# Kernel optimization log

Measured on AMD Instinct MI355X. Metric: run time of the kernel, lower is better.

Reference implementation:

```python
import jax, jax.numpy as jnp
import numpy as np

EPS = 1e-8
CUTOFF = 7.0
B, A, EPG = 128, 100, 2048
N, E = B * A, B * EPG
LAT, HID, FCH, NRBF, NTYPES, NT = 256, 128, 512, 16, 100, 50


def _lattice(lengths, angles):
    # pymatgen-style lattice_params_to_matrix; angles in degrees. -> [B,3,3] rows are a,b,c vectors
    a, b, c = lengths[:, 0], lengths[:, 1], lengths[:, 2]
    al, be, ga = (jnp.radians(angles[:, k]) for k in range(3))
    val = (jnp.cos(al) * jnp.cos(be) - jnp.cos(ga)) / (jnp.sin(al) * jnp.sin(be))
    gs = jnp.arccos(jnp.clip(val, -1.0, 1.0))
    z = jnp.zeros_like(a)
    va = jnp.stack([a * jnp.sin(be), z, a * jnp.cos(be)], -1)
    vb = jnp.stack([-b * jnp.sin(al) * jnp.cos(gs), b * jnp.sin(al) * jnp.sin(gs), b * jnp.cos(al)], -1)
    vc = jnp.stack([z, z, c], -1)
    return jnp.stack([va, vb, vc], 1)


def setup_inputs() -> dict:
    rng = np.random.default_rng(0)
    # sorted-per-graph edge list with i != j (so no_iden_mask is all-true)
    i = rng.integers(0, A, (B, EPG))
    j = (i + rng.integers(1, A, (B, EPG))) % A
    order = np.argsort(i * A + j, axis=1, kind='stable')
    i = np.take_along_axis(i, order, 1)
    j = np.take_along_axis(j, order, 1)
    goff = (np.arange(B) * A)[:, None]
    edge_index = np.stack([(j + goff).reshape(-1), (i + goff).reshape(-1)]).astype(np.int32)  # [2,E], row0=j(src), row1=i(dst)
    to_jimages = rng.integers(-1, 2, (E, 3)).astype(np.int32)
    batch = np.repeat(np.arange(B), A).astype(np.int32)
    num_atoms = np.full((B,), A, np.int32)
    atom_types = rng.integers(0, NTYPES, (N,)).astype(np.int32)
    time_steps = rng.integers(0, NT, (B,)).astype(np.int32)

    ks = jax.random.split(jax.random.key(0), 12)
    f32 = jnp.float32
    inp = dict(
        latents=jax.random.normal(ks[0], (B, LAT), f32),
        gt_frac_coords=jax.random.uniform(ks[1], (N, 3), f32),
        lengths=8.0 + 4.0 * jax.random.uniform(ks[2], (B, 3), f32),
        angles=90.0 + 8.0 * (jax.random.uniform(ks[3], (B, 3), f32) - 0.5),
        coord_noise=jax.random.normal(ks[4], (N, 3), f32),
        sigmas=jnp.exp(jnp.linspace(np.log(0.01), np.log(10.0), NT)).astype(f32),
        atom_emb=jax.random.normal(ks[5], (NTYPES, HID), f32),
        rbf_W=0.05 * jax.random.normal(ks[6], (NRBF, HID), f32),
        rbf_b=jnp.zeros((HID,), f32),
        bb_W=0.1 * jax.random.normal(ks[7], (HID, HID), f32),
        bb_b=jnp.zeros((HID,), f32),
        sc_W0=0.05 * jax.random.normal(ks[8], (LAT + HID, FCH), f32),
        sc_b0=jnp.zeros((FCH,), f32),
        sc_W1=0.05 * jax.random.normal(ks[9], (FCH, FCH), f32),
        sc_b1=jnp.zeros((FCH,), f32),
        sc_W2=0.05 * jax.random.normal(ks[10], (FCH, 1), f32),
        sc_b2=jnp.zeros((1,), f32),
        num_atoms=jnp.asarray(num_atoms),
        atom_types=jnp.asarray(atom_types),
        batch=jnp.asarray(batch),
        edge_index=jnp.asarray(edge_index),
        to_jimages=jnp.asarray(to_jimages),
        time_steps=jnp.asarray(time_steps),
    )
    return inp


def reference(latents, gt_frac_coords, lengths, angles, coord_noise, sigmas,
              atom_emb, rbf_W, rbf_b, bb_W, bb_b,
              sc_W0, sc_b0, sc_W1, sc_b1, sc_W2, sc_b2,
              num_atoms, atom_types, batch, edge_index, to_jimages, time_steps):
    seg_sum = jax.ops.segment_sum
    L = _lattice(lengths, angles)            # [B,3,3]
    Linv = jnp.linalg.inv(L)
    Ln, Lni = L[batch], Linv[batch]          # per-node lattice [N,3,3]
    cart_gt = jnp.einsum('ni,nij->nj', gt_frac_coords, Ln)
    sig_node = sigmas[time_steps][batch][:, None]              # [N,1]
    pert = cart_gt + sig_node * coord_noise
    # correct_cart_coords: wrap back into unit cell
    frac_p = jnp.einsum('ni,nij->nj', pert, Lni) % 1.0
    pert = jnp.einsum('ni,nij->nj', frac_p, Ln)
    jn, iN = edge_index[0], edge_index[1]
    offs = jnp.einsum('ei,eij->ej', to_jimages.astype(pert.dtype), L[batch[jn]])
    dvec = pert[iN] - pert[jn] - offs                           # [E,3]
    dist = jnp.linalg.norm(dvec, axis=-1)
    # backbone: atom-type embeddings + Gaussian RBF edge MLP -> [E,HID]
    mus = jnp.linspace(0.0, CUTOFF, rbf_W.shape[0]).astype(pert.dtype)
    rbf = jnp.exp(-10.0 * (dist[:, None] - mus) ** 2)
    h = atom_emb[atom_types]
    ef = jax.nn.silu((h[jn] + h[iN] + rbf @ rbf_W + rbf_b) @ bb_W + bb_b)
    # latents repeat_interleave(num_multi_edge_per_graph) == gather by edge's graph id
    ef = jnp.concatenate([ef, latents[batch[jn]]], axis=1)      # [E, HID+LAT]
    hh = jax.nn.relu(ef @ sc_W0 + sc_b0)
    hh = jax.nn.relu(hh @ sc_W1 + sc_b1)
    scores = hh @ sc_W2 + sc_b2                                 # [E,1]
    # align_gt_cart_coords: minimum-image gt coords relative to perturbed coords
    frac_gt = jnp.einsum('ni,nij->nj', cart_gt, Lni)
    fd = frac_gt - frac_p
    fd = fd - jnp.round(fd)
    aligned = pert + jnp.einsum('ni,nij->nj', fd, Ln)
    gt_dvec = aligned[iN] - aligned[jn] - offs
    gt_d = jnp.linalg.norm(gt_dvec, axis=-1, keepdims=True)
    pd = dist[:, None]
    gt_scores = gt_d - pd
    # per_node loss: group multi-edges by contiguous (i,j) runs
    start = jnp.concatenate([jnp.ones((1,), bool), (iN[1:] != iN[:-1]) | (jn[1:] != jn[:-1])])
    seg = jnp.cumsum(start.astype(jnp.int32)) - 1               # [E], < E segments
    cnt = seg_sum(jnp.ones((E,), pert.dtype), seg, num_segments=E)
    c = jnp.maximum(cnt, 1.0)
    sv = scores * dvec / (pd + EPS)
    gv = gt_scores * dvec / (pd + EPS)
    sE = seg_sum(sv, seg, num_segments=E) / c[:, None]
    gE = seg_sum(gv, seg, num_segments=E) / c[:, None]
    recv = jnp.round(seg_sum(iN.astype(pert.dtype), seg, num_segments=E) / c).astype(jnp.int32)
    sN = seg_sum(sE, recv, num_segments=N)                      # scores_per_node_pos [N,3]
    gN = seg_sum(gE, recv, num_segments=N)
    sq = (sN - gN / sig_node) ** 2
    na = num_atoms.astype(pert.dtype)[:, None]
    score_loss = (seg_sum(sq, batch, num_segments=B) / na).mean()
    # pbc symmetry regularizer
    preds = pert + sN / sig_node
    center = seg_sum(preds, batch, num_segments=B) / na
    dc = preds - center[batch]
    pbs = (jnp.abs(dc[:, 0].max() + dc[:, 0].min())
           + jnp.abs(dc[:, 1].max() + dc[:, 1].min())
           + jnp.abs(dc[:, 2].max() + dc[:, 2].min()))
    return (score_loss, pbs)
```

## Files before the change

### kernel.cpp

```cpp
#include <hip/hip_runtime.h>
#include <hip/hip_bf16.h>

namespace {
constexpr int Bb = 128, Nn = 12800, Ee = 262144;
constexpr int LAT = 256, HID = 128, FCH = 512, NRBF = 16;
constexpr int TE = 64;
constexpr int TSTRIDE = 1040;

constexpr int WS_L      = 0;
constexpr int WS_LI     = 1152;
constexpr int WS_SIG    = 2304;
constexpr int WS_RBFW2  = 2432;
constexpr int WS_CVEC   = 4480;
constexpr int WS_HB     = 4608;
constexpr int WS_LATP   = 17408;
constexpr int WS_PERT   = 82944;
constexpr int WS_ALIGN  = 121344;
constexpr int WS_SN     = 159744;
constexpr int WS_GN     = 198144;
constexpr int WS_PREDS  = 236544;
constexpr int WS_BSUM   = 274944;
constexpr int WS_CENTER = 275328;
constexpr int WS_MINMAX = 275712;
constexpr int WS_W0T_F  = 276000;
constexpr int WS_W1T_F  = 308768;
}

typedef short bf16x8 __attribute__((ext_vector_type(8)));
typedef float f32x4 __attribute__((ext_vector_type(4)));

static __device__ __forceinline__ unsigned short f2bf(float f) {
  unsigned int u = __float_as_uint(f);
  unsigned int r = (u + 0x7fffu + ((u >> 16) & 1u)) >> 16;
  return (unsigned short)r;
}
static __device__ __forceinline__ unsigned int pk2bf(float a, float b) {
  unsigned int r;
  asm("v_cvt_pk_bf16_f32 %0, %1, %2" : "=v"(r) : "v"(a), "v"(b));
  return r;
}
static __device__ __forceinline__ float fastrcp(float x) {
  return __builtin_amdgcn_rcpf(x);
}

static __device__ __forceinline__ void atomicMaxFloat(float* addr, float val) {
  int* ai = reinterpret_cast<int*>(addr);
  int old = *ai;
  while (__int_as_float(old) < val) {
    int assumed = old;
    old = atomicCAS(ai, assumed, __float_as_int(val));
    if (old == assumed) break;
  }
}
static __device__ __forceinline__ void atomicMinFloat(float* addr, float val) {
  int* ai = reinterpret_cast<int*>(addr);
  int old = *ai;
  while (__int_as_float(old) > val) {
    int assumed = old;
    old = atomicCAS(ai, assumed, __float_as_int(val));
    if (old == assumed) break;
  }
}

__global__ __launch_bounds__(256) void k_pre(
    const float* lengths, const float* angles, const float* sigmas, const int* tsteps,
    const float* aemb, const float* bbW, const float* rbfW, const float* rbfb,
    const float* bbb, const float* latents, const float* scW0, const float* scb0,
    const float* scW1, unsigned short* w0t, unsigned short* w1t, float* ws) {
  const int blk = blockIdx.x, t = threadIdx.x;
  if (blk < 304) {
    int gid = blk * 256 + t;
    if (gid < 2 * Nn * 3) ws[WS_SN + gid] = 0.f;
    else if (gid < 2 * Nn * 3 + 2 * Bb * 3) ws[WS_BSUM + (gid - 2 * Nn * 3)] = 0.f;
    else if (gid < 2 * Nn * 3 + 2 * Bb * 3 + 3) ws[WS_MINMAX + (gid - 2 * Nn * 3 - 2 * Bb * 3)] = -3.0e38f;
    else if (gid < 2 * Nn * 3 + 2 * Bb * 3 + 6) ws[WS_MINMAX + (gid - 2 * Nn * 3 - 2 * Bb * 3)] = 3.0e38f;
  } else if (blk == 304) {
    int b = t;
    if (b >= Bb) return;
    float a = lengths[b * 3 + 0], bl = lengths[b * 3 + 1], c = lengths[b * 3 + 2];
    const float d2r = 0.017453292519943295f;
    float al = angles[b * 3 + 0] * d2r, be = angles[b * 3 + 1] * d2r, ga = angles[b * 3 + 2] * d2r;
    float ca = cosf(al), cb = cosf(be), cg = cosf(ga), sa = sinf(al), sb = sinf(be);
    float val = (ca * cb - cg) / (sa * sb);
    val = fminf(1.f, fmaxf(-1.f, val));
    float gs = acosf(val);
    float L[3][3];
    L[0][0] = a * sb;              L[0][1] = 0.f;                L[0][2] = a * cb;
    L[1][0] = -bl * sa * cosf(gs); L[1][1] = bl * sa * sinf(gs); L[1][2] = bl * ca;
    L[2][0] = 0.f;                 L[2][1] = 0.f;                L[2][2] = c;
    float det = L[0][0] * (L[1][1] * L[2][2] - L[1][2] * L[2][1])
              - L[0][1] * (L[1][0] * L[2][2] - L[1][2] * L[2][0])
              + L[0][2] * (L[1][0] * L[2][1] - L[1][1] * L[2][0]);
    float id = 1.f / det;
    float inv[3][3];
    inv[0][0] =  (L[1][1]*L[2][2] - L[1][2]*L[2][1]) * id;
    inv[0][1] = -(L[0][1]*L[2][2] - L[0][2]*L[2][1]) * id;
    inv[0][2] =  (L[0][1]*L[1][2] - L[0][2]*L[1][1]) * id;
    inv[1][0] = -(L[1][0]*L[2][2] - L[1][2]*L[2][0]) * id;
    inv[1][1] =  (L[0][0]*L[2][2] - L[0][2]*L[2][0]) * id;
    inv[1][2] = -(L[0][0]*L[1][2] - L[0][2]*L[1][0]) * id;
    inv[2][0] =  (L[1][0]*L[2][1] - L[1][1]*L[2][0]) * id;
    inv[2][1] = -(L[0][0]*L[2][1] - L[0][1]*L[2][0]) * id;
    inv[2][2] =  (L[0][0]*L[1][1] - L[0][1]*L[1][0]) * id;
    for (int i = 0; i < 3; ++i)
      for (int j = 0; j < 3; ++j) {
        ws[WS_L + b * 9 + i * 3 + j] = L[i][j];
        ws[WS_LI + b * 9 + i * 3 + j] = inv[i][j];
      }
    ws[WS_SIG + b] = sigmas[tsteps[b]];
  } else if (blk < 405) {
    int tile = blk - 305;
    if (t < HID) {
      float acc = 0.f;
      for (int k = 0; k < HID; ++k) acc += aemb[tile * HID + k] * bbW[k * HID + t];
      ws[WS_HB + tile * HID + t] = acc;
    }
  } else if (blk == 405) {
    if (t < HID) {
      float accs[NRBF];
#pragma unroll
      for (int k = 0; k < NRBF; ++k) accs[k] = 0.f;
      float accb = 0.f;
      for (int m = 0; m < HID; ++m) {
        float w = bbW[m * HID + t];
#pragma unroll
        for (int k = 0; k < NRBF; ++k) accs[k] += rbfW[k * HID + m] * w;
        accb += rbfb[m] * w;
      }
#pragma unroll
      for (int k = 0; k < NRBF; ++k) ws[WS_RBFW2 + k * HID + t] = accs[k];
      ws[WS_CVEC + t] = accb + bbb[t];
    }
  } else if (blk < 534) {
    int b = blk - 406;
    __shared__ float lat[LAT];
    lat[t] = latents[b * LAT + t];
    __syncthreads();
    int c0 = 2 * t;
    float a0 = 0.f, a1 = 0.f;
    for (int m = 0; m < LAT; ++m) {
      float2 w = *reinterpret_cast<const float2*>(scW0 + (HID + m) * FCH + c0);
      float lm = lat[m];
      a0 += lm * w.x;
      a1 += lm * w.y;
    }
    ws[WS_LATP + b * FCH + c0] = a0 + scb0[c0];
    ws[WS_LATP + b * FCH + c0 + 1] = a1 + scb0[c0 + 1];
  } else if (blk < 790) {
    int tid = (blk - 534) * 256 + t;
    int col = tid & 511, k = tid >> 9;
    int id = (((col >> 4) * 4 + (k >> 5)) * 64 + ((k & 31) >> 3) * 16 + (col & 15)) * 8 + (k & 7);
    w0t[id] = f2bf(scW0[tid]);
  } else {
    int tid = (blk - 790) * 256 + t;
    int col = tid & 511, k = tid >> 9;
    int id = (((col >> 4) * 16 + (k >> 5)) * 64 + ((k & 31) >> 3) * 16 + (col & 15)) * 8 + (k & 7);
    w1t[id] = f2bf(scW1[tid]);
  }
}

__global__ void k_node(const float* frac, const float* noise, const int* batch, float* ws) {
  int n = blockIdx.x * blockDim.x + threadIdx.x;
  if (n >= Nn) return;
  int b = batch[n];
  float L[9], Li[9];
#pragma unroll
  for (int i = 0; i < 9; ++i) { L[i] = ws[WS_L + b * 9 + i]; Li[i] = ws[WS_LI + b * 9 + i]; }
  float f0 = frac[n * 3], f1 = frac[n * 3 + 1], f2 = frac[n * 3 + 2];
  float cg[3], p0[3], fp[3], pe[3], fg[3], fd[3];
#pragma unroll
  for (int j = 0; j < 3; ++j) cg[j] = f0 * L[j] + f1 * L[3 + j] + f2 * L[6 + j];
  float sig = ws[WS_SIG + b];
#pragma unroll
  for (int j = 0; j < 3; ++j) p0[j] = cg[j] + sig * noise[n * 3 + j];
#pragma unroll
  for (int j = 0; j < 3; ++j) {
    float v = p0[0] * Li[j] + p0[1] * Li[3 + j] + p0[2] * Li[6 + j];
    fp[j] = v - floorf(v);
  }
#pragma unroll
  for (int j = 0; j < 3; ++j) pe[j] = fp[0] * L[j] + fp[1] * L[3 + j] + fp[2] * L[6 + j];
#pragma unroll
  for (int j = 0; j < 3; ++j) fg[j] = cg[0] * Li[j] + cg[1] * Li[3 + j] + cg[2] * Li[6 + j];
#pragma unroll
  for (int j = 0; j < 3; ++j) { float d = fg[j] - fp[j]; fd[j] = d - rintf(d); }
#pragma unroll
  for (int j = 0; j < 3; ++j) {
    ws[WS_PERT + n * 3 + j] = pe[j];
    ws[WS_ALIGN + n * 3 + j] = pe[j] + fd[0] * L[j] + fd[1] * L[3 + j] + fd[2] * L[6 + j];
  }
}

__global__ __launch_bounds__(512, 4) void k_edge(
    const int* ei, const int* toj, const int* batch, const int* atype,
    const unsigned short* w0t, const unsigned short* w1t,
    const float* scb1, const float* scW2, const float* scb2, float* ws) {
  __shared__ __align__(16) char s_hh_b[64 * TSTRIDE];
  __shared__ float s_dvec[TE][3];
  __shared__ float s_dist[TE], s_gtd[TE];
  __shared__ int s_tj[TE], s_ti[TE];
  __shared__ float s_wsum[8][TE];

  char* s_ef_b = s_hh_b;
  float* s_rbfw2 = (float*)(s_hh_b + 16640);
  float* s_cvec  = (float*)(s_hh_b + 24832);
  float* s_rbfE  = (float*)(s_hh_b + 25344);

  const int t = threadIdx.x;
  const int e0 = blockIdx.x * TE;
  const int b0 = batch[ei[e0]];

  {
    const float4* src = (const float4*)(ws + WS_RBFW2);
    float4* dst = (float4*)s_rbfw2;
    dst[t] = src[t];
    if (t < 32) ((float4*)s_cvec)[t] = ((const float4*)(ws + WS_CVEC))[t];
  }
  if (t < TE) {
    int e = e0 + t;
    int jn = ei[e], iN = ei[Ee + e];
    int b = batch[jn];
    float tx = (float)toj[e * 3], ty = (float)toj[e * 3 + 1], tz = (float)toj[e * 3 + 2];
    const float* L = ws + WS_L + b * 9;
    float dv[3], gv[3];
#pragma unroll
    for (int j = 0; j < 3; ++j) {
      float off = tx * L[j] + ty * L[3 + j] + tz * L[6 + j];
      dv[j] = ws[WS_PERT + iN * 3 + j] - ws[WS_PERT + jn * 3 + j] - off;
      gv[j] = ws[WS_ALIGN + iN * 3 + j] - ws[WS_ALIGN + jn * 3 + j] - off;
    }
    float dist = sqrtf(dv[0] * dv[0] + dv[1] * dv[1] + dv[2] * dv[2]);
    float gtd = sqrtf(gv[0] * gv[0] + gv[1] * gv[1] + gv[2] * gv[2]);
#pragma unroll
    for (int j = 0; j < 3; ++j) s_dvec[t][j] = dv[j];
    s_dist[t] = dist;
    s_gtd[t] = gtd;
    s_tj[t] = atype[jn]; s_ti[t] = atype[iN];
    const float step = 7.0f / 15.0f;
#pragma unroll
    for (int k = 0; k < NRBF; ++k) {
      float d = dist - (float)k * step;
      s_rbfE[t * NRBF + k] = __expf(-10.f * d * d);
    }
  }
  __syncthreads();

  {
    int e = t >> 3;
    int c0 = (t & 7) * 16;
    int tj = s_tj[e], ti = s_ti[e];
    float4 rb4[4];
#pragma unroll
    for (int q = 0; q < 4; ++q) rb4[q] = ((const float4*)(s_rbfE + e * NRBF))[q];
    float rb[NRBF] = {rb4[0].x, rb4[0].y, rb4[0].z, rb4[0].w,
                      rb4[1].x, rb4[1].y, rb4[1].z, rb4[1].w,
                      rb4[2].x, rb4[2].y, rb4[2].z, rb4[2].w,
                      rb4[3].x, rb4[3].y, rb4[3].z, rb4[3].w};
    float4 z4[4];
#pragma unroll
    for (int q = 0; q < 4; ++q) {
      float4 a = *(const float4*)(ws + WS_HB + tj * HID + c0 + q * 4);
      float4 bq = *(const float4*)(ws + WS_HB + ti * HID + c0 + q * 4);
      float4 cv = ((const float4*)s_cvec)[c0 / 4 + q];
      z4[q].x = a.x + bq.x + cv.x; z4[q].y = a.y + bq.y + cv.y;
      z4[q].z = a.z + bq.z + cv.z; z4[q].w = a.w + bq.w + cv.w;
    }
#pragma unroll
    for (int k = 0; k < NRBF; ++k) {
      float rbk = rb[k];
#pragma unroll
      for (int q = 0; q < 4; ++q) {
        float4 wv4 = ((const float4*)s_rbfw2)[k * 32 + c0 / 4 + q];
        z4[q].x += rbk * wv4.x; z4[q].y += rbk * wv4.y;
        z4[q].z += rbk * wv4.z; z4[q].w += rbk * wv4.w;
      }
    }
    float sv[16];
#pragma unroll
    for (int q = 0; q < 4; ++q) {
      sv[q * 4 + 0] = z4[q].x * fastrcp(1.f + __expf(-z4[q].x));
      sv[q * 4 + 1] = z4[q].y * fastrcp(1.f + __expf(-z4[q].y));
      sv[q * 4 + 2] = z4[q].z * fastrcp(1.f + __expf(-z4[q].z));
      sv[q * 4 + 3] = z4[q].w * fastrcp(1.f + __expf(-z4[q].w));
    }
    unsigned int w[8];
#pragma unroll
    for (int p = 0; p < 8; ++p) w[p] = pk2bf(sv[2 * p], sv[2 * p + 1]);
    int eT = e >> 4, el = e & 15;
#pragma unroll
    for (int o = 0; o < 2; ++o) {
      int hid = c0 + 8 * o;
      int kt = hid >> 5;
      int oct = (hid & 31) >> 3;
      int addr = (kt * 4 + eT) * TSTRIDE + (el + 16 * oct) * 16;
      uint4 val = {w[4 * o + 0], w[4 * o + 1], w[4 * o + 2], w[4 * o + 3]};
      *(uint4*)(s_ef_b + addr) = val;
    }
  }
  __syncthreads();

  const int lane = t & 63;
  const int wv = t >> 6;
  const int el = lane & 15;
  const int q  = lane >> 4;

  {
    f32x4 acc[4][4];
#pragma unroll
    for (int m = 0; m < 4; ++m)
#pragma unroll
      for (int n = 0; n < 4; ++n) acc[m][n] = (f32x4){0.f, 0.f, 0.f, 0.f};
    const unsigned short* w0base = w0t + (size_t)(wv * 4) * 4 * 512 + lane * 8;
#pragma unroll
    for (int kt = 0; kt < 4; ++kt) {
      bf16x8 aw[4];
#pragma unroll
      for (int m = 0; m < 4; ++m)
        aw[m] = *(const bf16x8*)(w0base + (size_t)(m * 4 + kt) * 512);
      bf16x8 bf[4];
#pragma unroll
      for (int n = 0; n < 4; ++n)
        bf[n] = *(const bf16x8*)(s_ef_b + (kt * 4 + n) * TSTRIDE + lane * 16);
      __builtin_amdgcn_s_setprio(1);
#pragma unroll
      for (int n = 0; n < 4; ++n)
#pragma unroll
        for (int m = 0; m < 4; ++m)
          acc[m][n] = __builtin_amdgcn_mfma_f32_16x16x32_bf16(aw[m], bf[n], acc[m][n], 0, 0, 0);
      __builtin_amdgcn_s_setprio(0);
    }
    __syncthreads();
#pragma unroll
    for (int m = 0; m < 4; ++m) {
      float4 lp = *(const float4*)(ws + WS_LATP + b0 * FCH + wv * 64 + m * 16 + q * 4);
#pragma unroll
      for (int n = 0; n < 4; ++n) {
        f32x4 v = acc[m][n];
        float h0 = fmaxf(v[0] + lp.x, 0.f);
        float h1 = fmaxf(v[1] + lp.y, 0.f);
        float h2 = fmaxf(v[2] + lp.z, 0.f);
        float h3 = fmaxf(v[3] + lp.w, 0.f);
        uint2 val = {pk2bf(h0, h1), pk2bf(h2, h3)};
        int kT = wv * 2 + (m >> 1);
        int oct = (m & 1) * 2 + (q >> 1);
        int addr = (kT * 4 + n) * TSTRIDE + (el + 16 * oct) * 16 + (q & 1) * 8;
        *(uint2*)(s_hh_b + addr) = val;
      }
    }
  }
  __syncthreads();

  {
    f32x4 acc[4][4];
#pragma unroll
    for (int m = 0; m < 4; ++m)
#pragma unroll
      for (int n = 0; n < 4; ++n) acc[m][n] = (f32x4){0.f, 0.f, 0.f, 0.f};
    const unsigned short* w1base = w1t + (size_t)(wv * 4) * 16 * 512 + lane * 8;
#pragma unroll 4
    for (int kt = 0; kt < 16; ++kt) {
      bf16x8 aw[4];
#pragma unroll
      for (int m = 0; m < 4; ++m)
        aw[m] = *(const bf16x8*)(w1base + (size_t)(m * 16 + kt) * 512);
      bf16x8 bf[4];
#pragma unroll
      for (int n = 0; n < 4; ++n)
        bf[n] = *(const bf16x8*)(s_hh_b + (kt * 4 + n) * TSTRIDE + lane * 16);
      __builtin_amdgcn_s_setprio(1);
#pragma unroll
      for (int n = 0; n < 4; ++n)
#pragma unroll
        for (int m = 0; m < 4; ++m)
          acc[m][n] = __builtin_amdgcn_mfma_f32_16x16x32_bf16(aw[m], bf[n], acc[m][n], 0, 0, 0);
      __builtin_amdgcn_s_setprio(0);
    }
    float p[4] = {0.f, 0.f, 0.f, 0.f};
#pragma unroll
    for (int m = 0; m < 4; ++m) {
      int colb = wv * 64 + m * 16 + q * 4;
      float4 b1v = *(const float4*)(scb1 + colb);
      float4 w2v = *(const float4*)(scW2 + colb);
#pragma unroll
      for (int n = 0; n < 4; ++n) {
        f32x4 v = acc[m][n];
        p[n] += fmaxf(v[0] + b1v.x, 0.f) * w2v.x;
        p[n] += fmaxf(v[1] + b1v.y, 0.f) * w2v.y;
        p[n] += fmaxf(v[2] + b1v.z, 0.f) * w2v.z;
        p[n] += fmaxf(v[3] + b1v.w, 0.f) * w2v.w;
      }
    }
#pragma unroll
    for (int n = 0; n < 4; ++n) {
      float x = p[n];
      x += __shfl_xor(x, 16);
      x += __shfl_xor(x, 32);
      p[n] = x;
    }
    if (lane < 16) {
#pragma unroll
      for (int n = 0; n < 4; ++n) s_wsum[wv][n * 16 + el] = p[n];
    }
  }
  __syncthreads();

  if (t < TE) {
    int e = e0 + t;
    float score = scb2[0];
#pragma unroll
    for (int w = 0; w < 8; ++w) score += s_wsum[w][t];
    int jn = ei[e], iN = ei[Ee + e];
    int s = e;
    while (s > 0 && ei[s - 1] == jn && ei[Ee + s - 1] == iN) --s;
    int en = e;
    while (en + 1 < Ee && ei[en + 1] == jn && ei[Ee + en + 1] == iN) ++en;
    float invc = fastrcp((float)(en - s + 1));
    float dist = s_dist[t];
    float rden = fastrcp(dist + 1e-8f);
    float gts = s_gtd[t] - dist;
#pragma unroll
    for (int j = 0; j < 3; ++j) {
      float dir = s_dvec[t][j] * rden;
      atomicAdd(&ws[WS_SN + iN * 3 + j], score * dir * invc);
      atomicAdd(&ws[WS_GN + iN * 3 + j], gts * dir * invc);
    }
  }
}

__global__ void k_node2(const int* batch, float* ws) {
  int n = blockIdx.x * blockDim.x + threadIdx.x;
  if (n >= Nn) return;
  int b = batch[n];
  float sig = ws[WS_SIG + b];
#pragma unroll
  for (int j = 0; j < 3; ++j) {
    float s = ws[WS_SN + n * 3 + j], g = ws[WS_GN + n * 3 + j];
    float d = s - g / sig;
    atomicAdd(&ws[WS_BSUM + b * 3 + j], d * d);
    float pr = ws[WS_PERT + n * 3 + j] + s / sig;
    ws[WS_PREDS + n * 3 + j] = pr;
    atomicAdd(&ws[WS_CENTER + b * 3 + j], pr);
  }
}

__global__ void k_minmax(const int* batch, const int* num_atoms, float* ws) {
  int n = blockIdx.x * blockDim.x + threadIdx.x;
  int lane = threadIdx.x & 63, wid = threadIdx.x >> 6;
  float mx[3], mn[3];
  if (n < Nn) {
    int b = batch[n];
    float na = (float)num_atoms[b];
#pragma unroll
    for (int j = 0; j < 3; ++j) {
      float v = ws[WS_PREDS + n * 3 + j] - ws[WS_CENTER + b * 3 + j] / na;
      mx[j] = v; mn[j] = v;
    }
  } else {
#pragma unroll
    for (int j = 0; j < 3; ++j) { mx[j] = -3.0e38f; mn[j] = 3.0e38f; }
  }
#pragma unroll
  for (int off = 32; off >= 1; off >>= 1) {
#pragma unroll
    for (int j = 0; j < 3; ++j) {
      mx[j] = fmaxf(mx[j], __shfl_xor(mx[j], off));
      mn[j] = fminf(mn[j], __shfl_xor(mn[j], off));
    }
  }
  __shared__ float smx[4][3], smn[4][3];
  if (lane == 0) {
#pragma unroll
    for (int j = 0; j < 3; ++j) { smx[wid][j] = mx[j]; smn[wid][j] = mn[j]; }
  }
  __syncthreads();
  if (threadIdx.x == 0) {
#pragma unroll
    for (int j = 0; j < 3; ++j) {
      float M = fmaxf(fmaxf(smx[0][j], smx[1][j]), fmaxf(smx[2][j], smx[3][j]));
      float m = fminf(fminf(smn[0][j], smn[1][j]), fminf(smn[2][j], smn[3][j]));
      atomicMaxFloat(&ws[WS_MINMAX + j], M);
      atomicMinFloat(&ws[WS_MINMAX + 3 + j], m);
    }
  }
}

__global__ void k_final(const int* num_atoms, const float* ws, float* out) {
  int t = threadIdx.x;
  float loss = 0.f;
  if (t < Bb) {
    float na = (float)num_atoms[t];
    loss = (ws[WS_BSUM + t * 3] + ws[WS_BSUM + t * 3 + 1] + ws[WS_BSUM + t * 3 + 2]) / na;
  }
#pragma unroll
  for (int off = 32; off >= 1; off >>= 1) loss += __shfl_xor(loss, off);
  __shared__ float s2[2];
  if ((t & 63) == 0) s2[t >> 6] = loss;
  __syncthreads();
  if (t == 0) {
    float L = (s2[0] + s2[1]) / (3.0f * (float)Bb);
    float pbs = fabsf(ws[WS_MINMAX + 0] + ws[WS_MINMAX + 3]) +
                fabsf(ws[WS_MINMAX + 1] + ws[WS_MINMAX + 4]) +
                fabsf(ws[WS_MINMAX + 2] + ws[WS_MINMAX + 5]);
    out[0] = L;
    out[1] = pbs;
  }
}

extern "C" void kernel_launch(void* const* d_in, const int* in_sizes, int n_in,
                              void* d_out, int out_size, void* d_ws, size_t ws_size,
                              hipStream_t stream) {
  const float* latents = (const float*)d_in[0];
  const float* gtf     = (const float*)d_in[1];
  const float* lengths = (const float*)d_in[2];
  const float* angles  = (const float*)d_in[3];
  const float* noise   = (const float*)d_in[4];
  const float* sigmas  = (const float*)d_in[5];
  const float* aemb    = (const float*)d_in[6];
  const float* rbfW    = (const float*)d_in[7];
  const float* rbfb    = (const float*)d_in[8];
  const float* bbW     = (const float*)d_in[9];
  const float* bbb     = (const float*)d_in[10];
  const float* scW0    = (const float*)d_in[11];
  const float* scb0    = (const float*)d_in[12];
  const float* scW1    = (const float*)d_in[13];
  const float* scb1    = (const float*)d_in[14];
  const float* scW2    = (const float*)d_in[15];
  const float* scb2    = (const float*)d_in[16];
  const int* num_atoms = (const int*)d_in[17];
  const int* atype     = (const int*)d_in[18];
  const int* batch     = (const int*)d_in[19];
  const int* ei        = (const int*)d_in[20];
  const int* toj       = (const int*)d_in[21];
  const int* tsteps    = (const int*)d_in[22];
  float* ws = (float*)d_ws;
  float* out = (float*)d_out;
  unsigned short* w0t = (unsigned short*)(ws + WS_W0T_F);
  unsigned short* w1t = (unsigned short*)(ws + WS_W1T_F);

  hipLaunchKernelGGL(k_pre, dim3(1814), dim3(256), 0, stream,
                     lengths, angles, sigmas, tsteps, aemb, bbW, rbfW, rbfb, bbb,
                     latents, scW0, scb0, scW1, w0t, w1t, ws);
  hipLaunchKernelGGL(k_node, dim3(50), dim3(256), 0, stream, gtf, noise, batch, ws);
  hipLaunchKernelGGL(k_edge, dim3(Ee / TE), dim3(512), 0, stream,
                     ei, toj, batch, atype, w0t, w1t, scb1, scW2, scb2, ws);
  hipLaunchKernelGGL(k_node2, dim3(50), dim3(256), 0, stream, batch, ws);
  hipLaunchKernelGGL(k_minmax, dim3(50), dim3(256), 0, stream, batch, num_atoms, ws);
  hipLaunchKernelGGL(k_final, dim3(1), dim3(128), 0, stream, num_atoms, ws, out);
}
```

Before: 323.0 us.

## Fuse node kernel into pre kernel, vectorize weight transpose, double-buffer MFMA weight loads

```diff
diff --git a/kernel.cpp b/kernel.cpp
--- a/kernel.cpp
+++ b/kernel.cpp
@@ -27,6 +27,7 @@
 }
 
 typedef short bf16x8 __attribute__((ext_vector_type(8)));
+typedef unsigned short u16x8 __attribute__((ext_vector_type(8)));
 typedef float f32x4 __attribute__((ext_vector_type(4)));
 
 static __device__ __forceinline__ unsigned short f2bf(float f) {
@@ -41,6 +42,33 @@
 }
 static __device__ __forceinline__ float fastrcp(float x) {
   return __builtin_amdgcn_rcpf(x);
+}
+
+static __device__ __forceinline__ void make_lattice(
+    const float* lengths, const float* angles, int b, float L[9], float Li[9]) {
+  float a = lengths[b * 3 + 0], bl = lengths[b * 3 + 1], c = lengths[b * 3 + 2];
+  const float d2r = 0.017453292519943295f;
+  float al = angles[b * 3 + 0] * d2r, be = angles[b * 3 + 1] * d2r, ga = angles[b * 3 + 2] * d2r;
+  float ca = cosf(al), cb = cosf(be), cg = cosf(ga), sa = sinf(al), sb = sinf(be);
+  float val = (ca * cb - cg) / (sa * sb);
+  val = fminf(1.f, fmaxf(-1.f, val));
+  float gs = acosf(val);
+  L[0] = a * sb;              L[1] = 0.f;                L[2] = a * cb;
+  L[3] = -bl * sa * cosf(gs); L[4] = bl * sa * sinf(gs); L[5] = bl * ca;
+  L[6] = 0.f;                 L[7] = 0.f;                L[8] = c;
+  float det = L[0] * (L[4] * L[8] - L[5] * L[7])
+            - L[1] * (L[3] * L[8] - L[5] * L[6])
+            + L[2] * (L[3] * L[7] - L[4] * L[6]);
+  float id = 1.f / det;
+  Li[0] =  (L[4] * L[8] - L[5] * L[7]) * id;
+  Li[1] = -(L[1] * L[8] - L[2] * L[7]) * id;
+  Li[2] =  (L[1] * L[5] - L[2] * L[4]) * id;
+  Li[3] = -(L[3] * L[8] - L[5] * L[6]) * id;
+  Li[4] =  (L[0] * L[8] - L[2] * L[6]) * id;
+  Li[5] = -(L[0] * L[5] - L[2] * L[3]) * id;
+  Li[6] =  (L[3] * L[7] - L[4] * L[6]) * id;
+  Li[7] = -(L[0] * L[7] - L[1] * L[6]) * id;
+  Li[8] =  (L[0] * L[4] - L[1] * L[3]) * id;
 }
 
 static __device__ __forceinline__ void atomicMaxFloat(float* addr, float val) {
@@ -66,7 +94,8 @@
     const float* lengths, const float* angles, const float* sigmas, const int* tsteps,
     const float* aemb, const float* bbW, const float* rbfW, const float* rbfb,
     const float* bbb, const float* latents, const float* scW0, const float* scb0,
-    const float* scW1, unsigned short* w0t, unsigned short* w1t, float* ws) {
+    const float* scW1, const float* gtf, const float* noise, const int* batch,
+    const int* atype, unsigned short* w0t, unsigned short* w1t, float* ws) {
   const int blk = blockIdx.x, t = threadIdx.x;
   if (blk < 304) {
     int gid = blk * 256 + t;
@@ -77,36 +106,13 @@
   } else if (blk == 304) {
     int b = t;
     if (b >= Bb) return;
-    float a = lengths[b * 3 + 0], bl = lengths[b * 3 + 1], c = lengths[b * 3 + 2];
-    const float d2r = 0.017453292519943295f;
-    float al = angles[b * 3 + 0] * d2r, be = angles[b * 3 + 1] * d2r, ga = angles[b * 3 + 2] * d2r;
-    float ca = cosf(al), cb = cosf(be), cg = cosf(ga), sa = sinf(al), sb = sinf(be);
-    float val = (ca * cb - cg) / (sa * sb);
-    val = fminf(1.f, fmaxf(-1.f, val));
-    float gs = acosf(val);
-    float L[3][3];
-    L[0][0] = a * sb;              L[0][1] = 0.f;                L[0][2] = a * cb;
-    L[1][0] = -bl * sa * cosf(gs); L[1][1] = bl * sa * sinf(gs); L[1][2] = bl * ca;
-    L[2][0] = 0.f;                 L[2][1] = 0.f;                L[2][2] = c;
-    float det = L[0][0] * (L[1][1] * L[2][2] - L[1][2] * L[2][1])
-              - L[0][1] * (L[1][0] * L[2][2] - L[1][2] * L[2][0])
-              + L[0][2] * (L[1][0] * L[2][1] - L[1][1] * L[2][0]);
-    float id = 1.f / det;
-    float inv[3][3];
-    inv[0][0] =  (L[1][1]*L[2][2] - L[1][2]*L[2][1]) * id;
-    inv[0][1] = -(L[0][1]*L[2][2] - L[0][2]*L[2][1]) * id;
-    inv[0][2] =  (L[0][1]*L[1][2] - L[0][2]*L[1][1]) * id;
-    inv[1][0] = -(L[1][0]*L[2][2] - L[1][2]*L[2][0]) * id;
-    inv[1][1] =  (L[0][0]*L[2][2] - L[0][2]*L[2][0]) * id;
-    inv[1][2] = -(L[0][0]*L[1][2] - L[0][2]*L[1][0]) * id;
-    inv[2][0] =  (L[1][0]*L[2][1] - L[1][1]*L[2][0]) * id;
-    inv[2][1] = -(L[0][0]*L[2][1] - L[0][1]*L[2][0]) * id;
-    inv[2][2] =  (L[0][0]*L[1][1] - L[0][1]*L[1][0]) * id;
-    for (int i = 0; i < 3; ++i)
-      for (int j = 0; j < 3; ++j) {
-        ws[WS_L + b * 9 + i * 3 + j] = L[i][j];
-        ws[WS_LI + b * 9 + i * 3 + j] = inv[i][j];
-      }
+    float L[9], Li[9];
+    make_lattice(lengths, angles, b, L, Li);
+#pragma unroll
+    for (int i = 0; i < 9; ++i) {
+      ws[WS_L + b * 9 + i] = L[i];
+      ws[WS_LI + b * 9 + i] = Li[i];
+    }
     ws[WS_SIG + b] = sigmas[tsteps[b]];
   } else if (blk < 405) {
     int tile = blk - 305;
@@ -146,48 +152,55 @@
     }
     ws[WS_LATP + b * FCH + c0] = a0 + scb0[c0];
     ws[WS_LATP + b * FCH + c0 + 1] = a1 + scb0[c0 + 1];
-  } else if (blk < 790) {
-    int tid = (blk - 534) * 256 + t;
-    int col = tid & 511, k = tid >> 9;
-    int id = (((col >> 4) * 4 + (k >> 5)) * 64 + ((k & 31) >> 3) * 16 + (col & 15)) * 8 + (k & 7);
-    w0t[id] = f2bf(scW0[tid]);
+  } else if (blk < 566) {
+    int id8 = (blk - 534) * 256 + t;
+    int tile = id8 >> 6, lf = id8 & 63;
+    int colTile = tile >> 2, kTile = tile & 3;
+    int col = colTile * 16 + (lf & 15);
+    int kbase = kTile * 32 + (lf >> 4) * 8;
+    u16x8 v;
+#pragma unroll
+    for (int e = 0; e < 8; ++e) v[e] = f2bf(scW0[(kbase + e) * FCH + col]);
+    *(u16x8*)(w0t + id8 * 8) = v;
+  } else if (blk < 694) {
+    int id8 = (blk - 566) * 256 + t;
+    int tile = id8 >> 6, lf = id8 & 63;
+    int colTile = tile >> 4, kTile = tile & 15;
+    int col = colTile * 16 + (lf & 15);
+    int kbase = kTile * 32 + (lf >> 4) * 8;
+    u16x8 v;
+#pragma unroll
+    for (int e = 0; e < 8; ++e) v[e] = f2bf(scW1[(kbase + e) * FCH + col]);
+    *(u16x8*)(w1t + id8 * 8) = v;
   } else {
-    int tid = (blk - 790) * 256 + t;
-    int col = tid & 511, k = tid >> 9;
-    int id = (((col >> 4) * 16 + (k >> 5)) * 64 + ((k & 31) >> 3) * 16 + (col & 15)) * 8 + (k & 7);
-    w1t[id] = f2bf(scW1[tid]);
-  }
-}
-
-__global__ void k_node(const float* frac, const float* noise, const int* batch, float* ws) {
-  int n = blockIdx.x * blockDim.x + threadIdx.x;
-  if (n >= Nn) return;
-  int b = batch[n];
-  float L[9], Li[9];
-#pragma unroll
-  for (int i = 0; i < 9; ++i) { L[i] = ws[WS_L + b * 9 + i]; Li[i] = ws[WS_LI + b * 9 + i]; }
-  float f0 = frac[n * 3], f1 = frac[n * 3 + 1], f2 = frac[n * 3 + 2];
-  float cg[3], p0[3], fp[3], pe[3], fg[3], fd[3];
-#pragma unroll
-  for (int j = 0; j < 3; ++j) cg[j] = f0 * L[j] + f1 * L[3 + j] + f2 * L[6 + j];
-  float sig = ws[WS_SIG + b];
-#pragma unroll
-  for (int j = 0; j < 3; ++j) p0[j] = cg[j] + sig * noise[n * 3 + j];
-#pragma unroll
-  for (int j = 0; j < 3; ++j) {
-    float v = p0[0] * Li[j] + p0[1] * Li[3 + j] + p0[2] * Li[6 + j];
-    fp[j] = v - floorf(v);
-  }
-#pragma unroll
-  for (int j = 0; j < 3; ++j) pe[j] = fp[0] * L[j] + fp[1] * L[3 + j] + fp[2] * L[6 + j];
-#pragma unroll
-  for (int j = 0; j < 3; ++j) fg[j] = cg[0] * Li[j] + cg[1] * Li[3 + j] + cg[2] * Li[6 + j];
-#pragma unroll
-  for (int j = 0; j < 3; ++j) { float d = fg[j] - fp[j]; fd[j] = d - rintf(d); }
-#pragma unroll
-  for (int j = 0; j < 3; ++j) {
-    ws[WS_PERT + n * 3 + j] = pe[j];
-    ws[WS_ALIGN + n * 3 + j] = pe[j] + fd[0] * L[j] + fd[1] * L[3 + j] + fd[2] * L[6 + j];
+    int n = (blk - 694) * 256 + t;
+    if (n >= Nn) return;
+    int b = batch[n];
+    float L[9], Li[9];
+    make_lattice(lengths, angles, b, L, Li);
+    float sig = sigmas[tsteps[b]];
+    float f0 = gtf[n * 3], f1 = gtf[n * 3 + 1], f2 = gtf[n * 3 + 2];
+    float cg[3], p0[3], fp[3], pe[3], fg[3], fd[3];
+#pragma unroll
+    for (int j = 0; j < 3; ++j) cg[j] = f0 * L[j] + f1 * L[3 + j] + f2 * L[6 + j];
+#pragma unroll
+    for (int j = 0; j < 3; ++j) p0[j] = cg[j] + sig * noise[n * 3 + j];
+#pragma unroll
+    for (int j = 0; j < 3; ++j) {
+      float v = p0[0] * Li[j] + p0[1] * Li[3 + j] + p0[2] * Li[6 + j];
+      fp[j] = v - floorf(v);
+    }
+#pragma unroll
+    for (int j = 0; j < 3; ++j) pe[j] = fp[0] * L[j] + fp[1] * L[3 + j] + fp[2] * L[6 + j];
+#pragma unroll
+    for (int j = 0; j < 3; ++j) fg[j] = cg[0] * Li[j] + cg[1] * Li[3 + j] + cg[2] * Li[6 + j];
+#pragma unroll
+    for (int j = 0; j < 3; ++j) { float d = fg[j] - fp[j]; fd[j] = d - rintf(d); }
+#pragma unroll
+    for (int j = 0; j < 3; ++j) {
+      ws[WS_PERT + n * 3 + j] = pe[j];
+      ws[WS_ALIGN + n * 3 + j] = pe[j] + fd[0] * L[j] + fd[1] * L[3 + j] + fd[2] * L[6 + j];
+    }
   }
 }
 
@@ -210,6 +223,11 @@
   const int e0 = blockIdx.x * TE;
   const int b0 = batch[ei[e0]];
 
+  const int lane = t & 63;
+  const int wv = t >> 6;
+  const int el = lane & 15;
+  const int q  = lane >> 4;
+
   {
     const float4* src = (const float4*)(ws + WS_RBFW2);
     float4* dst = (float4*)s_rbfw2;
@@ -251,58 +269,64 @@
     int tj = s_tj[e], ti = s_ti[e];
     float4 rb4[4];
 #pragma unroll
-    for (int q = 0; q < 4; ++q) rb4[q] = ((const float4*)(s_rbfE + e * NRBF))[q];
+    for (int qq = 0; qq < 4; ++qq) rb4[qq] = ((const float4*)(s_rbfE + e * NRBF))[qq];
     float rb[NRBF] = {rb4[0].x, rb4[0].y, rb4[0].z, rb4[0].w,
                       rb4[1].x, rb4[1].y, rb4[1].z, rb4[1].w,
                       rb4[2].x, rb4[2].y, rb4[2].z, rb4[2].w,
                       rb4[3].x, rb4[3].y, rb4[3].z, rb4[3].w};
     float4 z4[4];
 #pragma unroll
-    for (int q = 0; q < 4; ++q) {
-      float4 a = *(const float4*)(ws + WS_HB + tj * HID + c0 + q * 4);
-      float4 bq = *(const float4*)(ws + WS_HB + ti * HID + c0 + q * 4);
-      float4 cv = ((const float4*)s_cvec)[c0 / 4 + q];
-      z4[q].x = a.x + bq.x + cv.x; z4[q].y = a.y + bq.y + cv.y;
-      z4[q].z = a.z + bq.z + cv.z; z4[q].w = a.w + bq.w + cv.w;
+    for (int qq = 0; qq < 4; ++qq) {
+      float4 a = *(const float4*)(ws + WS_HB + tj * HID + c0 + qq * 4);
+      float4 bq = *(const float4*)(ws + WS_HB + ti * HID + c0 + qq * 4);
+      float4 cv = ((const float4*)s_cvec)[c0 / 4 + qq];
+      z4[qq].x = a.x + bq.x + cv.x; z4[qq].y = a.y + bq.y + cv.y;
+      z4[qq].z = a.z + bq.z + cv.z; z4[qq].w = a.w + bq.w + cv.w;
     }
 #pragma unroll
     for (int k = 0; k < NRBF; ++k) {
       float rbk = rb[k];
 #pragma unroll
-      for (int q = 0; q < 4; ++q) {
-        float4 wv4 = ((const float4*)s_rbfw2)[k * 32 + c0 / 4 + q];
-        z4[q].x += rbk * wv4.x; z4[q].y += rbk * wv4.y;
-        z4[q].z += rbk * wv4.z; z4[q].w += rbk * wv4.w;
+      for (int qq = 0; qq < 4; ++qq) {
+        float4 wv4 = ((const float4*)s_rbfw2)[k * 32 + c0 / 4 + qq];
+        z4[qq].x += rbk * wv4.x; z4[qq].y += rbk * wv4.y;
+        z4[qq].z += rbk * wv4.z; z4[qq].w += rbk * wv4.w;
       }
     }
     float sv[16];
 #pragma unroll
-    for (int q = 0; q < 4; ++q) {
-      sv[q * 4 + 0] = z4[q].x * fastrcp(1.f + __expf(-z4[q].x));
-      sv[q * 4 + 1] = z4[q].y * fastrcp(1.f + __expf(-z4[q].y));
-      sv[q * 4 + 2] = z4[q].z * fastrcp(1.f + __expf(-z4[q].z));
-      sv[q * 4 + 3] = z4[q].w * fastrcp(1.f + __expf(-z4[q].w));
+    for (int qq = 0; qq < 4; ++qq) {
+      sv[qq * 4 + 0] = z4[qq].x * fastrcp(1.f + __expf(-z4[qq].x));
+      sv[qq * 4 + 1] = z4[qq].y * fastrcp(1.f + __expf(-z4[qq].y));
+      sv[qq * 4 + 2] = z4[qq].z * fastrcp(1.f + __expf(-z4[qq].z));
+      sv[qq * 4 + 3] = z4[qq].w * fastrcp(1.f + __expf(-z4[qq].w));
     }
     unsigned int w[8];
 #pragma unroll
     for (int p = 0; p < 8; ++p) w[p] = pk2bf(sv[2 * p], sv[2 * p + 1]);
-    int eT = e >> 4, el = e & 15;
+    int eT = e >> 4, elw = e & 15;
 #pragma unroll
     for (int o = 0; o < 2; ++o) {
       int hid = c0 + 8 * o;
       int kt = hid >> 5;
       int oct = (hid & 31) >> 3;
-      int addr = (kt * 4 + eT) * TSTRIDE + (el + 16 * oct) * 16;
+      int addr = (kt * 4 + eT) * TSTRIDE + (elw + 16 * oct) * 16;
       uint4 val = {w[4 * o + 0], w[4 * o + 1], w[4 * o + 2], w[4 * o + 3]};
       *(uint4*)(s_ef_b + addr) = val;
     }
   }
+
+  const unsigned short* w0base = w0t + (size_t)(wv * 4) * 4 * 512 + lane * 8;
+  bf16x8 cawA[4], cawB[4];
+#pragma unroll
+  for (int m = 0; m < 4; ++m) {
+    cawA[m] = *(const bf16x8*)(w0base + (size_t)(m * 4 + 0) * 512);
+    cawB[m] = *(const bf16x8*)(w0base + (size_t)(m * 4 + 1) * 512);
+  }
   __syncthreads();
 
-  const int lane = t & 63;
-  const int wv = t >> 6;
-  const int el = lane & 15;
-  const int q  = lane >> 4;
+  const unsigned short* w1base = w1t + (size_t)(wv * 4) * 16 * 512 + lane * 8;
+  bf16x8 dawA[4], dawB[4];
 
   {
     f32x4 acc[4][4];
@@ -310,25 +334,29 @@
     for (int m = 0; m < 4; ++m)
 #pragma unroll
       for (int n = 0; n < 4; ++n) acc[m][n] = (f32x4){0.f, 0.f, 0.f, 0.f};
-    const unsigned short* w0base = w0t + (size_t)(wv * 4) * 4 * 512 + lane * 8;
-#pragma unroll
-    for (int kt = 0; kt < 4; ++kt) {
-      bf16x8 aw[4];
-#pragma unroll
-      for (int m = 0; m < 4; ++m)
-        aw[m] = *(const bf16x8*)(w0base + (size_t)(m * 4 + kt) * 512);
-      bf16x8 bf[4];
-#pragma unroll
-      for (int n = 0; n < 4; ++n)
-        bf[n] = *(const bf16x8*)(s_ef_b + (kt * 4 + n) * TSTRIDE + lane * 16);
-      __builtin_amdgcn_s_setprio(1);
-#pragma unroll
-      for (int n = 0; n < 4; ++n)
-#pragma unroll
-        for (int m = 0; m < 4; ++m)
-          acc[m][n] = __builtin_amdgcn_mfma_f32_16x16x32_bf16(aw[m], bf[n], acc[m][n], 0, 0, 0);
-      __builtin_amdgcn_s_setprio(0);
-    }
+
+#define C_STEP(KT, CUR)                                                          \
+  {                                                                              \
+    bf16x8 bfv[4];                                                               \
+    _Pragma("unroll") for (int n = 0; n < 4; ++n)                                \
+        bfv[n] = *(const bf16x8*)(s_ef_b + ((KT) * 4 + n) * TSTRIDE + lane * 16);\
+    __builtin_amdgcn_s_setprio(1);                                               \
+    _Pragma("unroll") for (int n = 0; n < 4; ++n)                                \
+        _Pragma("unroll") for (int m = 0; m < 4; ++m)                            \
+            acc[m][n] = __builtin_amdgcn_mfma_f32_16x16x32_bf16(                 \
+                CUR[m], bfv[n], acc[m][n], 0, 0, 0);                             \
+    __builtin_amdgcn_s_setprio(0);                                               \
+    if ((KT) + 2 < 4) {                                                          \
+      _Pragma("unroll") for (int m = 0; m < 4; ++m)                              \
+          CUR[m] = *(const bf16x8*)(w0base + (size_t)(m * 4 + (KT) + 2) * 512);  \
+    }                                                                            \
+  }
+    C_STEP(0, cawA)
+    C_STEP(1, cawB)
+    C_STEP(2, cawA)
+    C_STEP(3, cawB)
+#undef C_STEP
+
     __syncthreads();
 #pragma unroll
     for (int m = 0; m < 4; ++m) {
@@ -348,6 +376,12 @@
       }
     }
   }
+
+#pragma unroll
+  for (int m = 0; m < 4; ++m) {
+    dawA[m] = *(const bf16x8*)(w1base + (size_t)(m * 16 + 0) * 512);
+    dawB[m] = *(const bf16x8*)(w1base + (size_t)(m * 16 + 1) * 512);
+  }
   __syncthreads();
 
   {
@@ -356,25 +390,33 @@
     for (int m = 0; m < 4; ++m)
 #pragma unroll
       for (int n = 0; n < 4; ++n) acc[m][n] = (f32x4){0.f, 0.f, 0.f, 0.f};
-    const unsigned short* w1base = w1t + (size_t)(wv * 4) * 16 * 512 + lane * 8;
-#pragma unroll 4
-    for (int kt = 0; kt < 16; ++kt) {
-      bf16x8 aw[4];
-#pragma unroll
-      for (int m = 0; m < 4; ++m)
-        aw[m] = *(const bf16x8*)(w1base + (size_t)(m * 16 + kt) * 512);
-      bf16x8 bf[4];
-#pragma unroll
-      for (int n = 0; n < 4; ++n)
-        bf[n] = *(const bf16x8*)(s_hh_b + (kt * 4 + n) * TSTRIDE + lane * 16);
-      __builtin_amdgcn_s_setprio(1);
-#pragma unroll
-      for (int n = 0; n < 4; ++n)
-#pragma unroll
-        for (int m = 0; m < 4; ++m)
-          acc[m][n] = __builtin_amdgcn_mfma_f32_16x16x32_bf16(aw[m], bf[n], acc[m][n], 0, 0, 0);
-      __builtin_amdgcn_s_setprio(0);
-    }
+
+#define D_STEP(KT, CUR)                                                          \
+  {                                                                              \
+    bf16x8 bfv[4];                                                               \
+    _Pragma("unroll") for (int n = 0; n < 4; ++n)                                \
+        bfv[n] = *(const bf16x8*)(s_hh_b + ((KT) * 4 + n) * TSTRIDE + lane * 16);\
+    __builtin_amdgcn_s_setprio(1);                                               \
+    _Pragma("unroll") for (int n = 0; n < 4; ++n)                                \
+        _Pragma("unroll") for (int m = 0; m < 4; ++m)                            \
+            acc[m][n] = __builtin_amdgcn_mfma_f32_16x16x32_bf16(                 \
+                CUR[m], bfv[n], acc[m][n], 0, 0, 0);                             \
+    __builtin_amdgcn_s_setprio(0);                                               \
+    if ((KT) + 2 < 16) {                                                         \
+      _Pragma("unroll") for (int m = 0; m < 4; ++m)                              \
+          CUR[m] = *(const bf16x8*)(w1base + (size_t)(m * 16 + (KT) + 2) * 512); \
+    }                                                                            \
+  }
+    D_STEP(0, dawA)  D_STEP(1, dawB)
+    D_STEP(2, dawA)  D_STEP(3, dawB)
+    D_STEP(4, dawA)  D_STEP(5, dawB)
+    D_STEP(6, dawA)  D_STEP(7, dawB)
+    D_STEP(8, dawA)  D_STEP(9, dawB)
+    D_STEP(10, dawA) D_STEP(11, dawB)
+    D_STEP(12, dawA) D_STEP(13, dawB)
+    D_STEP(14, dawA) D_STEP(15, dawB)
+#undef D_STEP
+
     float p[4] = {0.f, 0.f, 0.f, 0.f};
 #pragma unroll
     for (int m = 0; m < 4; ++m) {
@@ -537,10 +579,9 @@
   unsigned short* w0t = (unsigned short*)(ws + WS_W0T_F);
   unsigned short* w1t = (unsigned short*)(ws + WS_W1T_F);
 
-  hipLaunchKernelGGL(k_pre, dim3(1814), dim3(256), 0, stream,
+  hipLaunchKernelGGL(k_pre, dim3(744), dim3(256), 0, stream,
                      lengths, angles, sigmas, tsteps, aemb, bbW, rbfW, rbfb, bbb,
-                     latents, scW0, scb0, scW1, w0t, w1t, ws);
-  hipLaunchKernelGGL(k_node, dim3(50), dim3(256), 0, stream, gtf, noise, batch, ws);
+                     latents, scW0, scb0, scW1, gtf, noise, batch, atype, w0t, w1t, ws);
   hipLaunchKernelGGL(k_edge, dim3(Ee / TE), dim3(512), 0, stream,
                      ei, toj, batch, atype, w0t, w1t, scb1, scW2, scb2, ws);
   hipLaunchKernelGGL(k_node2, dim3(50), dim3(256), 0, stream, batch, ws);
```

New measurement: 351.9 us. 1.09x slower.
